# Performance work log

Hardware: AMD Instinct MI355X
Metric: run time of the kernel (lower is better)

The kernel has to match this reference:

```python
import jax, jax.numpy as jnp
import numpy as np

M, D = 1_000_000, 16   # source value store
N, K = 500_000, 8      # neurons, fan-in per neuron


def setup_inputs() -> dict:
    key = jax.random.key(0)
    k1, k2, k3, k4 = jax.random.split(key, 4)
    values = jax.random.normal(k1, (M, D), dtype=jnp.float32)
    idx = jax.random.randint(k2, (N, K), 0, M, dtype=jnp.int64)
    W = jax.random.normal(k3, (N, D, D), dtype=jnp.float32)
    b = jax.random.normal(k4, (N, D), dtype=jnp.float32)
    return {"values": values, "idx": idx, "W": W, "b": b}


def reference(values, idx, W, b):
    # GatherModule: irregular gather of per-neuron inputs -> [N, K, D]
    gathered = values[idx]
    # aggregate fan-in (weighted sum is realized by the per-neuron linear)
    s = gathered.sum(axis=1)            # [N, D]
    # per-neuron (non-shared) linear: y_n = W_n @ s_n + b_n
    y = jnp.einsum("nij,nj->ni", W, s) + b
    return jnp.tanh(y)
```

## Files before the change

kernel.cpp:

```cpp
#include <hip/hip_runtime.h>
#include <hip/hip_bf16.h>


#define D_DIM 16
#define K_FAN 8
#define NEUR_PER_BLOCK 16

__global__ __launch_bounds__(256)
void WeightedAtomLayer_55379308314866_kernel(
    const float* __restrict__ values,
    const int*   __restrict__ idx,
    const float* __restrict__ W,
    const float* __restrict__ b,
    float*       __restrict__ out,
    int N)
{
    __shared__ int   idx_sm[NEUR_PER_BLOCK][K_FAN];
    __shared__ float s_sm[NEUR_PER_BLOCK][D_DIM];

    const int t  = threadIdx.x;
    const int nl = t >> 4;
    const int i  = t & 15;
    const int n0 = blockIdx.x * NEUR_PER_BLOCK;
    const int n  = n0 + nl;

    if (t < NEUR_PER_BLOCK * K_FAN) {
        idx_sm[t >> 3][t & 7] = idx[n0 * K_FAN + t];
    }
    __syncthreads();

    float s = 0.0f;
    #pragma unroll
    for (int k = 0; k < K_FAN; ++k) {
        const long long row = (long long)idx_sm[nl][k];
        s += values[row * D_DIM + i];
    }
    s_sm[nl][i] = s;
    __syncthreads();

    const float4* Wv = (const float4*)(W + ((long long)n * (D_DIM * D_DIM)) + i * D_DIM);
    float acc = b[(long long)n * D_DIM + i];
    #pragma unroll
    for (int j4 = 0; j4 < 4; ++j4) {
        const float4 w = Wv[j4];
        acc += w.x * s_sm[nl][4 * j4 + 0];
        acc += w.y * s_sm[nl][4 * j4 + 1];
        acc += w.z * s_sm[nl][4 * j4 + 2];
        acc += w.w * s_sm[nl][4 * j4 + 3];
    }

    out[(long long)n * D_DIM + i] = tanhf(acc);
}

extern "C" void kernel_launch(void* const* d_in, const int* in_sizes, int n_in,
                              void* d_out, int out_size, void* d_ws, size_t ws_size,
                              hipStream_t stream) {
    const float* values = (const float*)d_in[0];
    const int*   idx    = (const int*)  d_in[1];
    const float* W      = (const float*)d_in[2];
    const float* b      = (const float*)d_in[3];
    float*       out    = (float*)d_out;

    const int N = in_sizes[3] / D_DIM;
    const int blocks = (N + NEUR_PER_BLOCK - 1) / NEUR_PER_BLOCK;

    WeightedAtomLayer_55379308314866_kernel<<<blocks, 256, 0, stream>>>(
        values, idx, W, b, out, N);
}
```

Before: 742.6 us.

## Split fused gather and matvec into two separate kernels via workspace

Splits the single fused kernel into a gather-sum kernel that writes the per-neuron sums to a workspace buffer, and a matvec kernel that reads them back and applies W, the bias and tanh. This likely aims to separate the random-access gather phase from the streaming W read so each kernel has a simpler access pattern. The cost is an extra global write and read of N*D floats plus a second launch. Bounds checks for partial blocks are also added.

Measured after the change: 775.3 us. 4.4% more time.

```diff
diff --git a/kernel.cpp b/kernel.cpp
--- a/kernel.cpp
+++ b/kernel.cpp
@@ -4,52 +4,73 @@
 
 #define D_DIM 16
 #define K_FAN 8
-#define NEUR_PER_BLOCK 16
+#define NPB 16
 
 __global__ __launch_bounds__(256)
-void WeightedAtomLayer_55379308314866_kernel(
-    const float* __restrict__ values,
-    const int*   __restrict__ idx,
-    const float* __restrict__ W,
-    const float* __restrict__ b,
-    float*       __restrict__ out,
-    int N)
+void gather_sum_kernel(const float* __restrict__ values,
+                       const int*   __restrict__ idx,
+                       float*       __restrict__ s_out,
+                       int N)
 {
-    __shared__ int   idx_sm[NEUR_PER_BLOCK][K_FAN];
-    __shared__ float s_sm[NEUR_PER_BLOCK][D_DIM];
+    __shared__ int idx_sm[NPB][K_FAN];
 
     const int t  = threadIdx.x;
     const int nl = t >> 4;
     const int i  = t & 15;
-    const int n0 = blockIdx.x * NEUR_PER_BLOCK;
+    const int n0 = blockIdx.x * NPB;
     const int n  = n0 + nl;
 
-    if (t < NEUR_PER_BLOCK * K_FAN) {
-        idx_sm[t >> 3][t & 7] = idx[n0 * K_FAN + t];
+    if (t < NPB * K_FAN) {
+        const int g = n0 * K_FAN + t;
+        idx_sm[t >> 3][t & 7] = (g < N * K_FAN) ? idx[g] : 0;
     }
     __syncthreads();
 
-    float s = 0.0f;
-    #pragma unroll
-    for (int k = 0; k < K_FAN; ++k) {
-        const long long row = (long long)idx_sm[nl][k];
-        s += values[row * D_DIM + i];
+    if (n < N) {
+        float s = 0.0f;
+        #pragma unroll
+        for (int k = 0; k < K_FAN; ++k) {
+            const long long row = (long long)idx_sm[nl][k];
+            s += values[row * D_DIM + i];
+        }
+        s_out[(long long)n * D_DIM + i] = s;
     }
-    s_sm[nl][i] = s;
+}
+
+__global__ __launch_bounds__(256)
+void matvec_kernel(const float* __restrict__ s_in,
+                   const float* __restrict__ W,
+                   const float* __restrict__ b,
+                   float*       __restrict__ out,
+                   int N)
+{
+    __shared__ float s_sm[NPB][D_DIM];
+
+    const int t  = threadIdx.x;
+    const int nl = t >> 4;
+    const int i  = t & 15;
+    const int n0 = blockIdx.x * NPB;
+    const int n  = n0 + nl;
+
+    {
+        const long long g = (long long)n0 * D_DIM + t;
+        s_sm[t >> 4][t & 15] = (g < (long long)N * D_DIM) ? s_in[g] : 0.0f;
+    }
     __syncthreads();
 
-    const float4* Wv = (const float4*)(W + ((long long)n * (D_DIM * D_DIM)) + i * D_DIM);
-    float acc = b[(long long)n * D_DIM + i];
-    #pragma unroll
-    for (int j4 = 0; j4 < 4; ++j4) {
-        const float4 w = Wv[j4];
-        acc += w.x * s_sm[nl][4 * j4 + 0];
-        acc += w.y * s_sm[nl][4 * j4 + 1];
-        acc += w.z * s_sm[nl][4 * j4 + 2];
-        acc += w.w * s_sm[nl][4 * j4 + 3];
+    if (n < N) {
+        const float4* Wv = (const float4*)(W + (long long)n * (D_DIM * D_DIM) + i * D_DIM);
+        float acc = b[(long long)n * D_DIM + i];
+        #pragma unroll
+        for (int j4 = 0; j4 < 4; ++j4) {
+            const float4 w = Wv[j4];
+            acc += w.x * s_sm[nl][4 * j4 + 0];
+            acc += w.y * s_sm[nl][4 * j4 + 1];
+            acc += w.z * s_sm[nl][4 * j4 + 2];
+            acc += w.w * s_sm[nl][4 * j4 + 3];
+        }
+        out[(long long)n * D_DIM + i] = tanhf(acc);
     }
-
-    out[(long long)n * D_DIM + i] = tanhf(acc);
 }
 
 extern "C" void kernel_launch(void* const* d_in, const int* in_sizes, int n_in,
@@ -60,10 +81,11 @@
     const float* W      = (const float*)d_in[2];
     const float* b      = (const float*)d_in[3];
     float*       out    = (float*)d_out;
+    float*       s_buf  = (float*)d_ws;
 
     const int N = in_sizes[3] / D_DIM;
-    const int blocks = (N + NEUR_PER_BLOCK - 1) / NEUR_PER_BLOCK;
+    const int blocks = (N + NPB - 1) / NPB;
 
-    WeightedAtomLayer_55379308314866_kernel<<<blocks, 256, 0, stream>>>(
-        values, idx, W, b, out, N);
+    gather_sum_kernel<<<blocks, 256, 0, stream>>>(values, idx, s_buf, N);
+    matvec_kernel<<<blocks, 256, 0, stream>>>(s_buf, W, b, out, N);
 }
```
